# Optimization experiments

Measured on AMD Instinct MI355X. Metric: run time of the kernel, lower is better.

The kernel has to match this reference:

```python
import jax, jax.numpy as jnp
import numpy as np

INPUT_DIM = 3
NUM_LEVELS = 16
LEVEL_DIM = 2
PER_LEVEL_SCALE = 2
BASE_RES = 16
MAX_PARAMS = 2 ** 19
BATCH = 2 ** 21

PRIMES = np.array([1, 2654435761, 805459861], dtype=np.uint32)
SORTED_BIN_MASK = np.triu(np.ones((INPUT_DIM + 1, INPUT_DIM), dtype=np.int32))


def _offsets():
    offs, off = [], 0
    for i in range(NUM_LEVELS):
        res = int(np.ceil(BASE_RES * PER_LEVEL_SCALE ** i))
        p = min(MAX_PARAMS, res ** INPUT_DIM)
        p = int(np.ceil(p / 32) * 32)
        off += p
        offs.append(off)
    return offs

OFFSETS = _offsets()  # cumulative, last entry = total table rows = 7114752


def setup_inputs() -> dict:
    key = jax.random.key(0)
    k1, k2 = jax.random.split(key)
    inputs = jax.random.uniform(k1, (BATCH, INPUT_DIM), dtype=jnp.float32)
    # xavier-uniform-ish init for the hash table
    total = OFFSETS[-1]
    a = float(np.sqrt(6.0 / (total + LEVEL_DIM)))
    embeddings = jax.random.uniform(k2, (total, LEVEL_DIM), dtype=jnp.float32,
                                    minval=-a, maxval=a)
    return {"inputs": inputs, "embeddings": embeddings}


def _fast_hash(ind_u32, hash_size):
    # ind_u32: [..., 3] uint32; uint32 multiply wraps mod 2^32 == (& 0xFFFFFFFF)
    h = ind_u32 * jnp.asarray(PRIMES)
    h = h[..., 0] ^ h[..., 1] ^ h[..., 2]
    return h % jnp.uint32(hash_size)


def _forward(inputs, embeddings):
    bin_mask_tbl = jnp.asarray(SORTED_BIN_MASK)  # [d+1, d]
    outs = []
    prev = 0
    for i in range(NUM_LEVELS):
        res = int(np.ceil(BASE_RES * PER_LEVEL_SCALE ** i))
        x = inputs * res                      # [B, d]
        xi = x.astype(jnp.int32)              # trunc == floor for x >= 0
        xf = x - jax.lax.stop_gradient(xi.astype(x.dtype))
        inds = jnp.argsort(xf, axis=-1)
        sorted_xf = jnp.take_along_axis(xf, inds, axis=-1)
        inv_inds = jnp.argsort(inds, axis=-1)
        bin_mask = bin_mask_tbl[:, inv_inds].transpose(1, 0, 2)  # [B, d+1, d]
        neigs = xi[:, None, :] + bin_mask                        # [B, d+1, d]
        hash_size = OFFSETS[i] - prev
        hids = _fast_hash(neigs.astype(jnp.uint32), hash_size).astype(jnp.int32) + prev
        feats = embeddings[hids]              # [B, d+1, level_dim] irregular gather
        # barycentric-style weights: consecutive diffs of sorted fracs padded with 0/1
        w_upper = jnp.concatenate([sorted_xf, jnp.ones_like(sorted_xf[..., :1])], axis=-1)
        w_lower = jnp.concatenate([jnp.zeros_like(sorted_xf[..., :1]), sorted_xf], axis=-1)
        w = (w_upper - w_lower)[..., None]    # [B, d+1, 1]
        outs.append(jnp.sum(feats * w, axis=-2))  # [B, level_dim]
        prev = OFFSETS[i]
    return jnp.concatenate(outs, axis=-1)     # [B, num_levels * level_dim]


def reference(inputs, embeddings):
    return _forward(inputs, embeddings)
```

## Files before the change

### kernel.cpp

```cpp
#include <hip/hip_runtime.h>
#include <hip/hip_fp16.h>
#include <stdint.h>


constexpr uint32_t kBatch   = 1u << 21;
constexpr uint32_t kQuarter = kBatch / 4u;
constexpr size_t   kWsNeed  = (size_t)kBatch * 16u * sizeof(uint32_t);

typedef float f32x2 __attribute__((ext_vector_type(2)));
typedef float f32x4 __attribute__((ext_vector_type(4)));

constexpr uint32_t PREV[16] = {
    0u, 4096u, 36864u, 299008u, 823296u, 1347584u, 1871872u, 2396160u,
    2920448u, 3444736u, 3969024u, 4493312u, 5017600u, 5541888u, 6066176u, 6590464u};
constexpr uint32_t MASK[16] = {
    4095u, 32767u, 262143u, 524287u, 524287u, 524287u, 524287u, 524287u,
    524287u, 524287u, 524287u, 524287u, 524287u, 524287u, 524287u, 524287u};

__device__ __forceinline__ void corner_hashes_weights(
    float x0, float x1, float x2, float res, uint32_t mask, uint32_t prev,
    uint32_t& g0, uint32_t& g1, uint32_t& g2, uint32_t& g3,
    float& sa, float& sb, float& sc)
{
    const float fx0 = x0 * res;
    const float fx1 = x1 * res;
    const float fx2 = x2 * res;
    const int i0 = (int)fx0;
    const int i1 = (int)fx1;
    const int i2 = (int)fx2;
    const float f0 = fx0 - (float)i0;
    const float f1 = fx1 - (float)i1;
    const float f2 = fx2 - (float)i2;

    const int r0 = (int)(f1 < f0) + (int)(f2 < f0);
    const int r1 = (int)(f0 < f1) + (int)(f2 < f1) + (int)(f0 == f1);
    const int r2 = (int)(f0 < f2) + (int)(f1 < f2) + (int)(f0 == f2) + (int)(f1 == f2);

    sa = fminf(fminf(f0, f1), f2);
    sc = fmaxf(fmaxf(f0, f1), f2);
    sb = __builtin_amdgcn_fmed3f(f0, f1, f2);

    const uint32_t A0 = (uint32_t)i0;
    const uint32_t A1 = A0 + 1u;
    const uint32_t B0 = (uint32_t)i1 * 2654435761u;
    const uint32_t B1 = ((uint32_t)i1 + 1u) * 2654435761u;
    const uint32_t C0 = (uint32_t)i2 * 805459861u;
    const uint32_t C1 = ((uint32_t)i2 + 1u) * 805459861u;

    const uint32_t h0 = A1 ^ B1 ^ C1;
    const uint32_t h1 = (r0 >= 1 ? A1 : A0) ^ (r1 >= 1 ? B1 : B0) ^ (r2 >= 1 ? C1 : C0);
    const uint32_t h2 = (r0 >= 2 ? A1 : A0) ^ (r1 >= 2 ? B1 : B0) ^ (r2 >= 2 ? C1 : C0);
    const uint32_t h3 = A0 ^ B0 ^ C0;

    g0 = (h0 & mask) + prev;
    g1 = (h1 & mask) + prev;
    g2 = (h2 & mask) + prev;
    g3 = (h3 & mask) + prev;
}

__device__ __forceinline__ uint32_t pack_f16x2(float x, float y) {
    const __half hx = __float2half(x);
    const __half hy = __float2half(y);
    return (uint32_t)__half_as_ushort(hx) | ((uint32_t)__half_as_ushort(hy) << 16);
}


__global__ __launch_bounds__(256) void gather16(
    const float* __restrict__ in,
    const float* __restrict__ emb,
    uint32_t* __restrict__ scr)
{
    __shared__ f32x2 tbl[4096];

    const uint32_t bid  = blockIdx.x;
    const uint32_t lvl  = bid >> 11;
    const uint32_t tid  = (bid & 2047u) * 256u + threadIdx.x;

    const float res = (float)(16u << lvl);
    const uint32_t mask = MASK[lvl];
    const uint32_t prev = PREV[lvl];
    uint32_t* slab = scr + (size_t)lvl * kBatch;

    f32x2 e[4][4];
    float sa[4], sb[4], sc[4];

    if (lvl == 0u) {
#pragma unroll
        for (uint32_t i = 0u; i < 16u; ++i) {
            const uint32_t r = threadIdx.x + 256u * i;
            tbl[r] = *reinterpret_cast<const f32x2*>(emb + 2u * r);
        }
        __syncthreads();

#pragma unroll
        for (int k = 0; k < 4; ++k) {
            const uint32_t b = tid + (uint32_t)k * kQuarter;
            const float x0 = __builtin_nontemporal_load(in + 3u * b + 0u);
            const float x1 = __builtin_nontemporal_load(in + 3u * b + 1u);
            const float x2 = __builtin_nontemporal_load(in + 3u * b + 2u);
            uint32_t g0, g1, g2, g3;
            corner_hashes_weights(x0, x1, x2, res, mask, prev, g0, g1, g2, g3,
                                  sa[k], sb[k], sc[k]);
            e[k][0] = tbl[g0];
            e[k][1] = tbl[g1];
            e[k][2] = tbl[g2];
            e[k][3] = tbl[g3];
        }
    } else {
#pragma unroll
        for (int k = 0; k < 4; ++k) {
            const uint32_t b = tid + (uint32_t)k * kQuarter;
            const float x0 = __builtin_nontemporal_load(in + 3u * b + 0u);
            const float x1 = __builtin_nontemporal_load(in + 3u * b + 1u);
            const float x2 = __builtin_nontemporal_load(in + 3u * b + 2u);
            uint32_t g0, g1, g2, g3;
            corner_hashes_weights(x0, x1, x2, res, mask, prev, g0, g1, g2, g3,
                                  sa[k], sb[k], sc[k]);
            e[k][0] = *reinterpret_cast<const f32x2*>(emb + 2u * g0);
            e[k][1] = *reinterpret_cast<const f32x2*>(emb + 2u * g1);
            e[k][2] = *reinterpret_cast<const f32x2*>(emb + 2u * g2);
            e[k][3] = *reinterpret_cast<const f32x2*>(emb + 2u * g3);
        }
        asm volatile(""
            : "+v"(e[0][0]), "+v"(e[0][1]), "+v"(e[0][2]), "+v"(e[0][3]),
              "+v"(e[1][0]), "+v"(e[1][1]), "+v"(e[1][2]), "+v"(e[1][3]),
              "+v"(e[2][0]), "+v"(e[2][1]), "+v"(e[2][2]), "+v"(e[2][3]),
              "+v"(e[3][0]), "+v"(e[3][1]), "+v"(e[3][2]), "+v"(e[3][3]));
    }

#pragma unroll
    for (int k = 0; k < 4; ++k) {
        const float w0 = sa[k];
        const float w1 = sb[k] - sa[k];
        const float w2 = sc[k] - sb[k];
        const float w3 = 1.0f - sc[k];
        const float vx = w0 * e[k][0].x + w1 * e[k][1].x + w2 * e[k][2].x + w3 * e[k][3].x;
        const float vy = w0 * e[k][0].y + w1 * e[k][1].y + w2 * e[k][2].y + w3 * e[k][3].y;
        const uint32_t b = tid + (uint32_t)k * kQuarter;
        __builtin_nontemporal_store(pack_f16x2(vx, vy), slab + b);
    }
}

__global__ __launch_bounds__(256) void transpose16(
    const uint32_t* __restrict__ scr,
    float* __restrict__ out)
{
    const uint32_t b = blockIdx.x * 256u + threadIdx.x;

    uint32_t p[16];
#pragma unroll
    for (int l = 0; l < 16; ++l)
        p[l] = __builtin_nontemporal_load(scr + (size_t)l * kBatch + b);

    float* o = out + (size_t)b * 32u;
#pragma unroll
    for (int q = 0; q < 8; ++q) {
        f32x4 t;
        t.x = __half2float(__ushort_as_half((unsigned short)(p[2 * q + 0] & 0xFFFFu)));
        t.y = __half2float(__ushort_as_half((unsigned short)(p[2 * q + 0] >> 16)));
        t.z = __half2float(__ushort_as_half((unsigned short)(p[2 * q + 1] & 0xFFFFu)));
        t.w = __half2float(__ushort_as_half((unsigned short)(p[2 * q + 1] >> 16)));
        *reinterpret_cast<f32x4*>(o + 4 * q) = t;
    }
}


__global__ __launch_bounds__(256) void pyramid_fwd_mono(
    const float* __restrict__ in,
    const float* __restrict__ emb,
    float* __restrict__ out)
{
    const uint32_t b = blockIdx.x * 256u + threadIdx.x;
    const float x0 = in[3u * b + 0u];
    const float x1 = in[3u * b + 1u];
    const float x2 = in[3u * b + 2u];

#pragma unroll
    for (int g = 0; g < 2; ++g) {
        float o8[16];
#pragma unroll
        for (int k = 0; k < 8; ++k) {
            const int lvl = g * 8 + k;
            const float res = (float)(16 << lvl);
            uint32_t g0, g1, g2, g3;
            float sa, sb, sc;
            corner_hashes_weights(x0, x1, x2, res, MASK[lvl], PREV[lvl],
                                  g0, g1, g2, g3, sa, sb, sc);
            const f32x2 e0 = *reinterpret_cast<const f32x2*>(emb + 2u * g0);
            const f32x2 e1 = *reinterpret_cast<const f32x2*>(emb + 2u * g1);
            const f32x2 e2 = *reinterpret_cast<const f32x2*>(emb + 2u * g2);
            const f32x2 e3 = *reinterpret_cast<const f32x2*>(emb + 2u * g3);
            const float w0 = sa, w1 = sb - sa, w2 = sc - sb, w3 = 1.0f - sc;
            o8[2 * k + 0] = w0 * e0.x + w1 * e1.x + w2 * e2.x + w3 * e3.x;
            o8[2 * k + 1] = w0 * e0.y + w1 * e1.y + w2 * e2.y + w3 * e3.y;
        }
        f32x4* o = reinterpret_cast<f32x4*>(out + (size_t)b * 32u + (size_t)g * 16u);
#pragma unroll
        for (int q = 0; q < 4; ++q) {
            f32x4 v;
            v.x = o8[4 * q + 0];
            v.y = o8[4 * q + 1];
            v.z = o8[4 * q + 2];
            v.w = o8[4 * q + 3];
            o[q] = v;
        }
    }
}


extern "C" void kernel_launch(void* const* d_in, const int* in_sizes, int n_in,
                              void* d_out, int out_size, void* d_ws, size_t ws_size,
                              hipStream_t stream) {
    const float* in  = (const float*)d_in[0];
    const float* emb = (const float*)d_in[1];
    float* out = (float*)d_out;

    dim3 tb(256u);

    if (ws_size >= kWsNeed) {
        uint32_t* scr = (uint32_t*)d_ws;
        dim3 gg(16u * 2048u);
        dim3 gt(kBatch / 256u);
        hipLaunchKernelGGL(gather16, gg, tb, 0, stream, in, emb, scr);
        hipLaunchKernelGGL(transpose16, gt, tb, 0, stream, scr, out);
    } else {
        dim3 grid(kBatch / 256u);
        hipLaunchKernelGGL(pyramid_fwd_mono, grid, tb, 0, stream, in, emb, out);
    }
}
```

Before: 680.3 us.

## Split coarse levels into persistent LDS-cached kernel, gather remaining levels separately

```diff
diff --git a/kernel.cpp b/kernel.cpp
--- a/kernel.cpp
+++ b/kernel.cpp
@@ -4,7 +4,6 @@
 
 
 constexpr uint32_t kBatch   = 1u << 21;
-constexpr uint32_t kQuarter = kBatch / 4u;
 constexpr size_t   kWsNeed  = (size_t)kBatch * 16u * sizeof(uint32_t);
 
 typedef float f32x2 __attribute__((ext_vector_type(2)));
@@ -64,17 +63,97 @@
     return (uint32_t)__half_as_ushort(hx) | ((uint32_t)__half_as_ushort(hy) << 16);
 }
 
-
-__global__ __launch_bounds__(256) void gather16(
+__device__ __forceinline__ float lo_h(uint32_t p) {
+    return __half2float(__ushort_as_half((unsigned short)(p & 0xFFFFu)));
+}
+__device__ __forceinline__ float hi_h(uint32_t p) {
+    return __half2float(__ushort_as_half((unsigned short)(p >> 16)));
+}
+
+
+__global__ __launch_bounds__(1024) void hybrid012(
     const float* __restrict__ in,
     const float* __restrict__ emb,
     uint32_t* __restrict__ scr)
 {
-    __shared__ f32x2 tbl[4096];
-
+    __shared__ uint32_t t0[4096];
+    __shared__ uint32_t t1[32768];
+
+    const uint32_t t = threadIdx.x;
+
+#pragma unroll
+    for (uint32_t i = 0u; i < 4u; ++i) {
+        const uint32_t r = t + 1024u * i;
+        const f32x2 v = *reinterpret_cast<const f32x2*>(emb + 2u * r);
+        t0[r] = pack_f16x2(v.x, v.y);
+    }
+#pragma unroll
+    for (uint32_t i = 0u; i < 32u; ++i) {
+        const uint32_t r = t + 1024u * i;
+        const f32x2 v = *reinterpret_cast<const f32x2*>(emb + 2u * (4096u + r));
+        t1[r] = pack_f16x2(v.x, v.y);
+    }
+    __syncthreads();
+
+    const uint32_t tid = blockIdx.x * 1024u + t;
+
+#pragma unroll 1
+    for (uint32_t k = 0u; k < 8u; ++k) {
+        const uint32_t b = tid + k * 262144u;
+        const float x0 = __builtin_nontemporal_load(in + 3u * b + 0u);
+        const float x1 = __builtin_nontemporal_load(in + 3u * b + 1u);
+        const float x2 = __builtin_nontemporal_load(in + 3u * b + 2u);
+
+        uint32_t g0, g1, g2, g3;
+        float sa2, sb2, sc2;
+        corner_hashes_weights(x0, x1, x2, 64.0f, 262143u, 36864u,
+                              g0, g1, g2, g3, sa2, sb2, sc2);
+        f32x2 e2a = *reinterpret_cast<const f32x2*>(emb + 2u * g0);
+        f32x2 e2b = *reinterpret_cast<const f32x2*>(emb + 2u * g1);
+        f32x2 e2c = *reinterpret_cast<const f32x2*>(emb + 2u * g2);
+        f32x2 e2d = *reinterpret_cast<const f32x2*>(emb + 2u * g3);
+
+        {
+            uint32_t l0, l1, l2, l3;
+            float sa, sb, sc;
+            corner_hashes_weights(x0, x1, x2, 16.0f, 4095u, 0u,
+                                  l0, l1, l2, l3, sa, sb, sc);
+            const uint32_t p0 = t0[l0], p1 = t0[l1], p2 = t0[l2], p3 = t0[l3];
+            const float w0 = sa, w1 = sb - sa, w2 = sc - sb, w3 = 1.0f - sc;
+            const float vx = w0 * lo_h(p0) + w1 * lo_h(p1) + w2 * lo_h(p2) + w3 * lo_h(p3);
+            const float vy = w0 * hi_h(p0) + w1 * hi_h(p1) + w2 * hi_h(p2) + w3 * hi_h(p3);
+            __builtin_nontemporal_store(pack_f16x2(vx, vy), scr + b);
+        }
+        {
+            uint32_t l0, l1, l2, l3;
+            float sa, sb, sc;
+            corner_hashes_weights(x0, x1, x2, 32.0f, 32767u, 0u,
+                                  l0, l1, l2, l3, sa, sb, sc);
+            const uint32_t p0 = t1[l0], p1 = t1[l1], p2 = t1[l2], p3 = t1[l3];
+            const float w0 = sa, w1 = sb - sa, w2 = sc - sb, w3 = 1.0f - sc;
+            const float vx = w0 * lo_h(p0) + w1 * lo_h(p1) + w2 * lo_h(p2) + w3 * lo_h(p3);
+            const float vy = w0 * hi_h(p0) + w1 * hi_h(p1) + w2 * hi_h(p2) + w3 * hi_h(p3);
+            __builtin_nontemporal_store(pack_f16x2(vx, vy), scr + (size_t)kBatch + b);
+        }
+
+        asm volatile("" : "+v"(e2a), "+v"(e2b), "+v"(e2c), "+v"(e2d));
+        const float w0 = sa2, w1 = sb2 - sa2, w2 = sc2 - sb2, w3 = 1.0f - sc2;
+        const float vx = w0 * e2a.x + w1 * e2b.x + w2 * e2c.x + w3 * e2d.x;
+        const float vy = w0 * e2a.y + w1 * e2b.y + w2 * e2c.y + w3 * e2d.y;
+        __builtin_nontemporal_store(pack_f16x2(vx, vy), scr + (size_t)2u * kBatch + b);
+    }
+}
+
+
+__global__ __launch_bounds__(256) void gather13(
+    const float* __restrict__ in,
+    const float* __restrict__ emb,
+    uint32_t* __restrict__ scr)
+{
     const uint32_t bid  = blockIdx.x;
-    const uint32_t lvl  = bid >> 11;
+    const uint32_t lvl  = 3u + (bid >> 11);
     const uint32_t tid  = (bid & 2047u) * 256u + threadIdx.x;
+    const uint32_t quarter = kBatch / 4u;
 
     const float res = (float)(16u << lvl);
     const uint32_t mask = MASK[lvl];
@@ -84,49 +163,26 @@
     f32x2 e[4][4];
     float sa[4], sb[4], sc[4];
 
-    if (lvl == 0u) {
-#pragma unroll
-        for (uint32_t i = 0u; i < 16u; ++i) {
-            const uint32_t r = threadIdx.x + 256u * i;
-            tbl[r] = *reinterpret_cast<const f32x2*>(emb + 2u * r);
-        }
-        __syncthreads();
-
-#pragma unroll
-        for (int k = 0; k < 4; ++k) {
-            const uint32_t b = tid + (uint32_t)k * kQuarter;
-            const float x0 = __builtin_nontemporal_load(in + 3u * b + 0u);
-            const float x1 = __builtin_nontemporal_load(in + 3u * b + 1u);
-            const float x2 = __builtin_nontemporal_load(in + 3u * b + 2u);
-            uint32_t g0, g1, g2, g3;
-            corner_hashes_weights(x0, x1, x2, res, mask, prev, g0, g1, g2, g3,
-                                  sa[k], sb[k], sc[k]);
-            e[k][0] = tbl[g0];
-            e[k][1] = tbl[g1];
-            e[k][2] = tbl[g2];
-            e[k][3] = tbl[g3];
-        }
-    } else {
-#pragma unroll
-        for (int k = 0; k < 4; ++k) {
-            const uint32_t b = tid + (uint32_t)k * kQuarter;
-            const float x0 = __builtin_nontemporal_load(in + 3u * b + 0u);
-            const float x1 = __builtin_nontemporal_load(in + 3u * b + 1u);
-            const float x2 = __builtin_nontemporal_load(in + 3u * b + 2u);
-            uint32_t g0, g1, g2, g3;
-            corner_hashes_weights(x0, x1, x2, res, mask, prev, g0, g1, g2, g3,
-                                  sa[k], sb[k], sc[k]);
-            e[k][0] = *reinterpret_cast<const f32x2*>(emb + 2u * g0);
-            e[k][1] = *reinterpret_cast<const f32x2*>(emb + 2u * g1);
-            e[k][2] = *reinterpret_cast<const f32x2*>(emb + 2u * g2);
-            e[k][3] = *reinterpret_cast<const f32x2*>(emb + 2u * g3);
-        }
-        asm volatile(""
-            : "+v"(e[0][0]), "+v"(e[0][1]), "+v"(e[0][2]), "+v"(e[0][3]),
-              "+v"(e[1][0]), "+v"(e[1][1]), "+v"(e[1][2]), "+v"(e[1][3]),
-              "+v"(e[2][0]), "+v"(e[2][1]), "+v"(e[2][2]), "+v"(e[2][3]),
-              "+v"(e[3][0]), "+v"(e[3][1]), "+v"(e[3][2]), "+v"(e[3][3]));
-    }
+#pragma unroll
+    for (int k = 0; k < 4; ++k) {
+        const uint32_t b = tid + (uint32_t)k * quarter;
+        const float x0 = __builtin_nontemporal_load(in + 3u * b + 0u);
+        const float x1 = __builtin_nontemporal_load(in + 3u * b + 1u);
+        const float x2 = __builtin_nontemporal_load(in + 3u * b + 2u);
+        uint32_t g0, g1, g2, g3;
+        corner_hashes_weights(x0, x1, x2, res, mask, prev, g0, g1, g2, g3,
+                              sa[k], sb[k], sc[k]);
+        e[k][0] = *reinterpret_cast<const f32x2*>(emb + 2u * g0);
+        e[k][1] = *reinterpret_cast<const f32x2*>(emb + 2u * g1);
+        e[k][2] = *reinterpret_cast<const f32x2*>(emb + 2u * g2);
+        e[k][3] = *reinterpret_cast<const f32x2*>(emb + 2u * g3);
+    }
+
+    asm volatile(""
+        : "+v"(e[0][0]), "+v"(e[0][1]), "+v"(e[0][2]), "+v"(e[0][3]),
+          "+v"(e[1][0]), "+v"(e[1][1]), "+v"(e[1][2]), "+v"(e[1][3]),
+          "+v"(e[2][0]), "+v"(e[2][1]), "+v"(e[2][2]), "+v"(e[2][3]),
+          "+v"(e[3][0]), "+v"(e[3][1]), "+v"(e[3][2]), "+v"(e[3][3]));
 
 #pragma unroll
     for (int k = 0; k < 4; ++k) {
@@ -136,7 +192,7 @@
         const float w3 = 1.0f - sc[k];
         const float vx = w0 * e[k][0].x + w1 * e[k][1].x + w2 * e[k][2].x + w3 * e[k][3].x;
         const float vy = w0 * e[k][0].y + w1 * e[k][1].y + w2 * e[k][2].y + w3 * e[k][3].y;
-        const uint32_t b = tid + (uint32_t)k * kQuarter;
+        const uint32_t b = tid + (uint32_t)k * quarter;
         __builtin_nontemporal_store(pack_f16x2(vx, vy), slab + b);
     }
 }
@@ -156,10 +212,10 @@
 #pragma unroll
     for (int q = 0; q < 8; ++q) {
         f32x4 t;
-        t.x = __half2float(__ushort_as_half((unsigned short)(p[2 * q + 0] & 0xFFFFu)));
-        t.y = __half2float(__ushort_as_half((unsigned short)(p[2 * q + 0] >> 16)));
-        t.z = __half2float(__ushort_as_half((unsigned short)(p[2 * q + 1] & 0xFFFFu)));
-        t.w = __half2float(__ushort_as_half((unsigned short)(p[2 * q + 1] >> 16)));
+        t.x = lo_h(p[2 * q + 0]);
+        t.y = hi_h(p[2 * q + 0]);
+        t.z = lo_h(p[2 * q + 1]);
+        t.w = hi_h(p[2 * q + 1]);
         *reinterpret_cast<f32x4*>(o + 4 * q) = t;
     }
 }
@@ -215,16 +271,13 @@
     const float* emb = (const float*)d_in[1];
     float* out = (float*)d_out;
 
-    dim3 tb(256u);
-
     if (ws_size >= kWsNeed) {
         uint32_t* scr = (uint32_t*)d_ws;
-        dim3 gg(16u * 2048u);
-        dim3 gt(kBatch / 256u);
-        hipLaunchKernelGGL(gather16, gg, tb, 0, stream, in, emb, scr);
-        hipLaunchKernelGGL(transpose16, gt, tb, 0, stream, scr, out);
+        hipLaunchKernelGGL(hybrid012, dim3(256u), dim3(1024u), 0, stream, in, emb, scr);
+        hipLaunchKernelGGL(gather13, dim3(13u * 2048u), dim3(256u), 0, stream, in, emb, scr);
+        hipLaunchKernelGGL(transpose16, dim3(kBatch / 256u), dim3(256u), 0, stream, scr, out);
     } else {
-        dim3 grid(kBatch / 256u);
-        hipLaunchKernelGGL(pyramid_fwd_mono, grid, tb, 0, stream, in, emb, out);
-    }
-}
+        hipLaunchKernelGGL(pyramid_fwd_mono, dim3(kBatch / 256u), dim3(256u), 0, stream,
+                           in, emb, out);
+    }
+}
```

After: 662.7 us (median of 2 runs). -2.6%, faster.
